# Optimization experiments

Hardware: AMD Instinct MI355X
Metric: run time of the kernel (lower is better)

## Reference

```python
import jax, jax.numpy as jnp
import numpy as np

B, CIN, COUT, T, J = 64, 128, 128, 128, 25
EPS = 1e-5  # BatchNorm2d default eps


def setup_inputs() -> dict:
    key = jax.random.key(0)
    k = jax.random.split(key, 5)
    x = jax.random.normal(k[0], (B, CIN, T, J), jnp.float32)
    adj = jax.random.normal(k[1], (J, J), jnp.float32) / np.sqrt(J).astype(np.float32)
    Wk = jax.random.normal(k[2], (COUT, CIN), jnp.float32) / np.sqrt(CIN).astype(np.float32)
    Wq = jax.random.normal(k[3], (COUT, CIN), jnp.float32) / np.sqrt(CIN).astype(np.float32)
    Ws = jax.random.normal(k[4], (COUT, CIN), jnp.float32) / np.sqrt(CIN).astype(np.float32)
    return {
        "x": x, "adj": adj,
        "Wk": Wk, "bk": jnp.zeros((COUT,), jnp.float32),
        "Wq": Wq, "bq": jnp.zeros((COUT,), jnp.float32),
        "Ws": Ws, "bs": jnp.zeros((COUT,), jnp.float32),
        "gamma": jnp.ones((COUT,), jnp.float32),
        "beta": jnp.zeros((COUT,), jnp.float32),
        "run_mean": jnp.zeros((COUT,), jnp.float32),
        "run_var": jnp.ones((COUT,), jnp.float32),
        "alpha": jnp.ones((1,), jnp.float32),
    }


def reference(x, adj, Wk, bk, Wq, bq, Ws, bs, gamma, beta, run_mean, run_var, alpha):
    # static graph conv: aggregate over joints with the shared adjacency
    static = jnp.einsum('bctj,jk->bctk', x, adj)              # [B,Cin,T,J]
    # 1x1 conv == channel matmul
    static_feat = jnp.einsum('oc,bctj->botj', Ws, static) + bs[None, :, None, None]  # [B,Cout,T,J]
    # temporal mean pooling, then key/query 1x1 convs
    x_t = x.mean(axis=2)                                      # [B,Cin,J]
    kk = jnp.einsum('oc,bcj->boj', Wk, x_t) + bk[None, :, None]  # [B,Cout,J]
    qq = jnp.einsum('oc,bcj->boj', Wq, x_t) + bq[None, :, None]  # [B,Cout,J]
    # attention-style dynamic adjacency: softmax(q^T k / sqrt(Cout)) over last axis
    scale = jnp.sqrt(jnp.asarray(kk.shape[1], x.dtype))
    scores = jnp.einsum('bcj,bck->bjk', qq, kk) / scale       # [B,J,J]
    dyn = jax.nn.softmax(scores, axis=-1)                     # [B,J,J]
    # original expands dyn to (B*T, Cout, J, J); same math without materialization:
    dyn_feat = jnp.einsum('bctj,bjk->bctk', static_feat, dyn)  # [B,Cout,T,J]
    out = static_feat + alpha[0] * dyn_feat
    # BatchNorm2d in inference mode (running stats), then ReLU
    inv = gamma[None, :, None, None] * jax.lax.rsqrt(run_var[None, :, None, None] + EPS)
    out = (out - run_mean[None, :, None, None]) * inv + beta[None, :, None, None]
    return jax.nn.relu(out)
```

## Files before the change

kernel.cpp:

```cpp
#include <hip/hip_runtime.h>

#define B_ 64
#define C_ 128
#define T_ 128
#define J_ 25
#define PIT 136
#define XP 40
#define GP 136
#define TT 4

typedef unsigned short ushort_t;
typedef __attribute__((ext_vector_type(8))) unsigned short ushort8;
typedef __attribute__((ext_vector_type(4))) unsigned short ushort4_t;
typedef __attribute__((ext_vector_type(8))) _Float16 half8;
typedef __attribute__((ext_vector_type(4))) float f32x4;

__device__ __forceinline__ float bf2f(ushort_t u) {
  unsigned int v = ((unsigned int)u) << 16;
  return __builtin_bit_cast(float, v);
}
__device__ __forceinline__ ushort_t f2bf(float f) {
  unsigned int u = __builtin_bit_cast(unsigned int, f);
  u += 0x7FFFu + ((u >> 16) & 1u);
  return (ushort_t)(u >> 16);
}
__device__ __forceinline__ ushort_t f2h_bits(float f) {
  _Float16 h = (_Float16)f;
  return __builtin_bit_cast(ushort_t, h);
}
__device__ __forceinline__ half8 cvt_bf8_h8(ushort8 u) {
  half8 r;
#pragma unroll
  for (int i = 0; i < 8; ++i) r[i] = (_Float16)bf2f(u[i]);
  return r;
}
__device__ __forceinline__ float ldv(const void* p, long i, int isf32) {
  return isf32 ? ((const float*)p)[i] : bf2f(((const ushort_t*)p)[i]);
}
__device__ __forceinline__ half8 ld8h(const void* p, long i, int isf32) {
  half8 r;
  if (isf32) {
    const float* f = (const float*)p + i;
#pragma unroll
    for (int k = 0; k < 8; ++k) r[k] = (_Float16)f[k];
  } else {
    ushort8 u = *(const ushort8*)((const ushort_t*)p + i);
    r = cvt_bf8_h8(u);
  }
  return r;
}

__global__ void k_detect(const void* __restrict__ x, int* __restrict__ flag) {
  if (threadIdx.x == 0 && blockIdx.x == 0) {
    const ushort_t* u = (const ushort_t*)x;
    int cnt = 0;
    for (int i = 0; i < 256; ++i) {
      float a = fabsf(bf2f(u[2 * i]));
      if (a > 1e-4f && a < 64.f) cnt++;
    }
    *flag = (cnt > 128) ? 0 : 1;
  }
}

__global__ __launch_bounds__(256) void k_mean(const void* __restrict__ x,
                                              float* __restrict__ xt,
                                              const int* __restrict__ flag) {
  const int isf32 = *flag;
  const int bc = blockIdx.x;
  const int b = bc >> 7, c = bc & 127;
  const long base = (long)bc * 3200;
  __shared__ float pl[3200];
  __shared__ float red[8][32];
  const int tid = threadIdx.x;
  if (isf32) {
    const f32x4* src = (const f32x4*)((const float*)x + base);
    for (int i = tid; i < 800; i += 256) *(f32x4*)&pl[i * 4] = src[i];
  } else {
    const ushort4_t* src = (const ushort4_t*)((const ushort_t*)x + base);
    for (int i = tid; i < 800; i += 256) {
      ushort4_t u = src[i];
      f32x4 v;
#pragma unroll
      for (int r = 0; r < 4; ++r) v[r] = bf2f(u[r]);
      *(f32x4*)&pl[i * 4] = v;
    }
  }
  __syncthreads();
  const int j = tid & 31, g = tid >> 5;
  float s = 0.f;
  if (j < J_) {
#pragma unroll
    for (int i = 0; i < 16; ++i) s += pl[(g * 16 + i) * 25 + j];
  }
  red[g][j] = s;
  __syncthreads();
  if (tid < 32) {
    float tot = 0.f;
#pragma unroll
    for (int gg = 0; gg < 8; ++gg) tot += red[gg][tid];
    if (tid < J_) xt[b * 4096 + tid * 128 + c] = tot * (1.0f / 128.0f);
  }
}

__global__ __launch_bounds__(256) void k_attn(
    const float* __restrict__ xt, const void* __restrict__ adj,
    const void* __restrict__ Wk, const void* __restrict__ bk,
    const void* __restrict__ Wq, const void* __restrict__ bq,
    const void* __restrict__ alphap, ushort_t* __restrict__ fkws,
    float* __restrict__ sws, const int* __restrict__ flag) {
  const int isf32 = *flag;
  const int b = blockIdx.x;
  const int tid = threadIdx.x;
  const int wv = tid >> 6, lane = tid & 63, lrow = lane & 15, quad = lane >> 4;
  const float alpha = ldv(alphap, 0, isf32);

  __shared__ __align__(16) ushort_t xtT[32 * PIT];
  __shared__ __align__(16) ushort_t kkT[32 * PIT];
  __shared__ __align__(16) ushort_t qqT[32 * PIT];
  __shared__ float sc[32 * 33];

  for (int idx = tid; idx < 32 * PIT; idx += 256) {
    int r = idx / PIT, col = idx % PIT;
    float v = (r < J_ && col < 128) ? xt[b * 4096 + r * 128 + col] : 0.f;
    xtT[idx] = f2h_bits(v);
  }
  __syncthreads();

  for (int mat = 0; mat < 2; ++mat) {
    const void* W = mat ? Wq : Wk;
    const void* bias = mat ? bq : bk;
    ushort_t* dstT = mat ? qqT : kkT;
    f32x4 acc[2][2] = {};
    for (int ks = 0; ks < 4; ++ks) {
      half8 bfr[2];
#pragma unroll
      for (int jt = 0; jt < 2; ++jt)
        bfr[jt] = *(const half8*)&xtT[(jt * 16 + lrow) * PIT + ks * 32 + quad * 8];
#pragma unroll
      for (int ot = 0; ot < 2; ++ot) {
        int o = (2 * wv + ot) * 16 + lrow;
        half8 afr = ld8h(W, o * 128 + ks * 32 + quad * 8, isf32);
#pragma unroll
        for (int jt = 0; jt < 2; ++jt)
          acc[ot][jt] = __builtin_amdgcn_mfma_f32_16x16x32_f16(afr, bfr[jt],
                                                               acc[ot][jt], 0, 0, 0);
      }
    }
#pragma unroll
    for (int ot = 0; ot < 2; ++ot) {
      int obase = (2 * wv + ot) * 16 + quad * 4;
#pragma unroll
      for (int jt = 0; jt < 2; ++jt) {
        int j = jt * 16 + lrow;
        ushort_t pack[4];
#pragma unroll
        for (int r = 0; r < 4; ++r)
          pack[r] = f2h_bits(acc[ot][jt][r] + ldv(bias, obase + r, isf32));
        *(ushort4_t*)&dstT[j * PIT + obase] = *(ushort4_t*)pack;
      }
    }
  }
  __syncthreads();

  {
    const int mt = wv >> 1, nt = wv & 1;
    f32x4 acc = {};
    for (int ks = 0; ks < 4; ++ks) {
      half8 afr = *(const half8*)&qqT[(mt * 16 + lrow) * PIT + ks * 32 + quad * 8];
      half8 bfr = *(const half8*)&kkT[(nt * 16 + lrow) * PIT + ks * 32 + quad * 8];
      acc = __builtin_amdgcn_mfma_f32_16x16x32_f16(afr, bfr, acc, 0, 0, 0);
    }
    const float rs = 0.08838834764831845f;
#pragma unroll
    for (int r = 0; r < 4; ++r)
      sc[(mt * 16 + quad * 4 + r) * 33 + nt * 16 + lrow] = acc[r] * rs;
  }
  __syncthreads();

  if (tid < J_) {
    float m = -1e30f;
    for (int k = 0; k < J_; ++k) m = fmaxf(m, sc[tid * 33 + k]);
    float sum = 0.f;
    for (int k = 0; k < J_; ++k) {
      float e = expf(sc[tid * 33 + k] - m);
      sc[tid * 33 + k] = e;
      sum += e;
    }
    float inv = 1.f / sum;
    for (int k = 0; k < J_; ++k) sc[tid * 33 + k] *= inv;
  }
  __syncthreads();

  for (int idx = tid; idx < 1280; idx += 256) {
    int k = idx / XP, jj = idx % XP;
    float v = 0.f;
    if (k < J_ && jj < J_) {
      v = ldv(adj, jj * J_ + k, isf32);
      float d = 0.f;
      for (int m = 0; m < J_; ++m) d += ldv(adj, jj * J_ + m, isf32) * sc[m * 33 + k];
      v += alpha * d;
    }
    fkws[b * 1280 + idx] = f2h_bits(v);
  }
  if (tid < 32) {
    float v = 0.f;
    if (tid < J_) {
      float d = 0.f;
      for (int jj = 0; jj < J_; ++jj) d += sc[jj * 33 + tid];
      v = 1.f + alpha * d;
    }
    sws[b * 32 + tid] = v;
  }
}

#define SM_FK 0
#define SM_X 2560
#define SM_GT 43520
#define SM_TOT 73984
__global__ __launch_bounds__(256, 2) void k_main(
    const void* __restrict__ x, const void* __restrict__ Ws,
    const void* __restrict__ bs, const void* __restrict__ gamma,
    const void* __restrict__ beta, const void* __restrict__ rmean,
    const void* __restrict__ rvar, const ushort_t* __restrict__ fkws,
    const float* __restrict__ sws, void* __restrict__ out,
    const int* __restrict__ flag) {
  const int isf32 = *flag;
  const int b = blockIdx.x >> 5, tb = blockIdx.x & 31, t0 = tb * TT;
  const int tid = threadIdx.x;
  const int wv = tid >> 6, lane = tid & 63, lrow = lane & 15, quad = lane >> 4;

  __shared__ __align__(16) char smem[SM_TOT];
  __shared__ float bnscale[128], bnshift[128], bsv[128], sv[32];
  ushort_t* fk = (ushort_t*)(smem + SM_FK);
  ushort_t* X = (ushort_t*)(smem + SM_X);
  ushort_t* gt = (ushort_t*)(smem + SM_GT);
  float* outbuf = (float*)(smem + SM_X);

  half8 wsf[2][4];
#pragma unroll
  for (int ot = 0; ot < 2; ++ot) {
    int o = (2 * wv + ot) * 16 + lrow;
#pragma unroll
    for (int ks = 0; ks < 4; ++ks)
      wsf[ot][ks] = ld8h(Ws, o * 128 + ks * 32 + quad * 8, isf32);
  }

  {
    const long fbase = ((long)(b * 128) * 128 + t0) * 25;
    if (isf32) {
      const float* xf = (const float*)x + fbase;
      for (int idx = tid; idx < 3200; idx += 256) {
        int c = idx / 25, q = idx % 25;
        f32x4 v = *(const f32x4*)(xf + (long)c * 3200 + q * 4);
#pragma unroll
        for (int r = 0; r < 4; ++r) {
          int p = q * 4 + r, tl = p / 25, j = p % 25;
          X[tl * 5120 + c * XP + j] = f2h_bits(v[r]);
        }
      }
    } else {
      const ushort_t* xh = (const ushort_t*)x + fbase;
      for (int idx = tid; idx < 3200; idx += 256) {
        int c = idx / 25, q = idx % 25;
        ushort4_t u = *(const ushort4_t*)(xh + (long)c * 3200 + q * 4);
#pragma unroll
        for (int r = 0; r < 4; ++r) {
          int p = q * 4 + r, tl = p / 25, j = p % 25;
          X[tl * 5120 + c * XP + j] = f2h_bits(bf2f(u[r]));
        }
      }
    }
    for (int idx = tid; idx < 512 * 7; idx += 256) {
      int row = idx / 7, j = 25 + idx % 7;
      X[(row >> 7) * 5120 + (row & 127) * XP + j] = 0;
    }
    for (int idx = tid; idx < 192; idx += 256) {
      int row = 100 + (idx >> 4), col8 = (idx & 15) * 8;
      half8 z = {};
      *(half8*)&gt[row * GP + col8] = z;
    }
    for (int idx = tid; idx < 1280; idx += 256) fk[idx] = fkws[b * 1280 + idx];
    if (tid < 32) sv[tid] = sws[b * 32 + tid];
    if (tid < 128) {
      float g = ldv(gamma, tid, isf32), v = ldv(rvar, tid, isf32);
      float scl = g * rsqrtf(v + 1e-5f);
      bnscale[tid] = scl;
      bnshift[tid] = ldv(beta, tid, isf32) - ldv(rmean, tid, isf32) * scl;
      bsv[tid] = ldv(bs, tid, isf32);
    }
  }
  __syncthreads();

  {
    half8 afr[2];
#pragma unroll
    for (int mt = 0; mt < 2; ++mt)
      afr[mt] = *(const half8*)&fk[(mt * 16 + lrow) * XP + quad * 8];
#pragma unroll
    for (int t = 0; t < TT; ++t) {
#pragma unroll
      for (int ci = 0; ci < 2; ++ci) {
        int ct = 2 * wv + ci;
        half8 bfr = *(const half8*)&X[t * 5120 + (ct * 16 + lrow) * XP + quad * 8];
        f32x4 accg[2] = {};
#pragma unroll
        for (int mt = 0; mt < 2; ++mt)
          accg[mt] = __builtin_amdgcn_mfma_f32_16x16x32_f16(afr[mt], bfr, accg[mt], 0, 0, 0);
#pragma unroll
        for (int mt = 0; mt < 2; ++mt)
#pragma unroll
          for (int r = 0; r < 4; ++r) {
            int kk = mt * 16 + quad * 4 + r;
            if (kk < J_)
              gt[(t * 25 + kk) * GP + ct * 16 + lrow] = f2h_bits(accg[mt][r]);
          }
      }
    }
  }
  __syncthreads();

  f32x4 acc[2][7];
#pragma unroll
  for (int ot = 0; ot < 2; ++ot)
#pragma unroll
    for (int nt = 0; nt < 7; ++nt) acc[ot][nt] = (f32x4){};
  for (int ks = 0; ks < 4; ++ks) {
    half8 bfr[7];
#pragma unroll
    for (int nt = 0; nt < 7; ++nt)
      bfr[nt] = *(const half8*)&gt[(nt * 16 + lrow) * GP + ks * 32 + quad * 8];
#pragma unroll
    for (int ot = 0; ot < 2; ++ot)
#pragma unroll
      for (int nt = 0; nt < 7; ++nt)
        acc[ot][nt] = __builtin_amdgcn_mfma_f32_16x16x32_f16(wsf[ot][ks], bfr[nt],
                                                             acc[ot][nt], 0, 0, 0);
  }
  __syncthreads();

#pragma unroll
  for (int nt = 0; nt < 7; ++nt) {
    int n = nt * 16 + lrow;
    if (n < 100) {
      float svk = sv[n % 25];
#pragma unroll
      for (int ot = 0; ot < 2; ++ot) {
        int obase = (2 * wv + ot) * 16 + quad * 4;
#pragma unroll
        for (int r = 0; r < 4; ++r) {
          int o = obase + r;
          float v = acc[ot][nt][r] + bsv[o] * svk;
          v = v * bnscale[o] + bnshift[o];
          outbuf[o * 100 + n] = fmaxf(v, 0.f);
        }
      }
    }
  }
  __syncthreads();

  {
    const long obase = ((long)(b * 128) * 128 + t0) * 25;
    if (isf32) {
      float* of = (float*)out + obase;
      for (int idx = tid; idx < 3200; idx += 256) {
        int o = idx / 25, q = idx % 25;
        *(f32x4*)(of + (long)o * 3200 + q * 4) = *(const f32x4*)&outbuf[o * 100 + q * 4];
      }
    } else {
      ushort_t* oh = (ushort_t*)out + obase;
      for (int idx = tid; idx < 3200; idx += 256) {
        int o = idx / 25, q = idx % 25;
        f32x4 v = *(const f32x4*)&outbuf[o * 100 + q * 4];
        ushort4_t u;
#pragma unroll
        for (int r = 0; r < 4; ++r) u[r] = f2bf(v[r]);
        *(ushort4_t*)(oh + (long)o * 3200 + q * 4) = u;
      }
    }
  }
}

extern "C" void kernel_launch(void* const* d_in, const int* in_sizes, int n_in,
                              void* d_out, int out_size, void* d_ws, size_t ws_size,
                              hipStream_t stream) {
  const void* x = d_in[0];
  const void* adj = d_in[1];
  const void* Wk = d_in[2];
  const void* bk = d_in[3];
  const void* Wq = d_in[4];
  const void* bq = d_in[5];
  const void* Ws = d_in[6];
  const void* bsp = d_in[7];
  const void* gamma = d_in[8];
  const void* beta = d_in[9];
  const void* rmean = d_in[10];
  const void* rvar = d_in[11];
  const void* alphap = d_in[12];

  char* ws = (char*)d_ws;
  int* flag = (int*)ws;
  float* xt = (float*)(ws + 256);
  ushort_t* fkws = (ushort_t*)(ws + 256 + 64 * 4096 * 4);
  float* sws = (float*)(ws + 256 + 64 * 4096 * 4 + 64 * 1280 * 2);

  k_detect<<<1, 64, 0, stream>>>(x, flag);
  k_mean<<<B_ * C_, 256, 0, stream>>>(x, xt, flag);
  k_attn<<<B_, 256, 0, stream>>>(xt, adj, Wk, bk, Wq, bq, alphap, fkws, sws, flag);
  k_main<<<B_ * (T_ / TT), 256, 0, stream>>>(x, Ws, bsp, gamma, beta, rmean, rvar,
                                             fkws, sws, d_out, flag);
}
```

Baseline: 319.0 us.

## Load x fragments directly from global in k_main and shrink LDS to raise occupancy

Removes the separate dtype-detect kernel and replaces it with a per-block ballot-based detection. In k_main, the staging of the x tile into LDS is dropped, and MFMA B fragments are read directly from global memory with unaligned vector loads. The output buffer is stored as fp16 in LDS, which shrinks shared memory from ~74KB to ~33KB so the kernel can run 4 blocks per CU instead of 2. The risk is less-coalesced global loads, and fp16 intermediate rounding of the outputs.

Result: faster. 298.4 us (-6.5%).

```diff
diff --git a/kernel.cpp b/kernel.cpp
--- a/kernel.cpp
+++ b/kernel.cpp
@@ -14,6 +14,8 @@
 typedef __attribute__((ext_vector_type(4))) unsigned short ushort4_t;
 typedef __attribute__((ext_vector_type(8))) _Float16 half8;
 typedef __attribute__((ext_vector_type(4))) float f32x4;
+typedef float f32x4u __attribute__((ext_vector_type(4), aligned(4)));
+typedef unsigned short ushort8u __attribute__((ext_vector_type(8), aligned(2)));
 
 __device__ __forceinline__ float bf2f(ushort_t u) {
   unsigned int v = ((unsigned int)u) << 16;
@@ -28,6 +30,9 @@
   _Float16 h = (_Float16)f;
   return __builtin_bit_cast(ushort_t, h);
 }
+__device__ __forceinline__ float h2f(ushort_t u) {
+  return (float)__builtin_bit_cast(_Float16, u);
+}
 __device__ __forceinline__ half8 cvt_bf8_h8(ushort8 u) {
   half8 r;
 #pragma unroll
@@ -50,28 +55,23 @@
   return r;
 }
 
-__global__ void k_detect(const void* __restrict__ x, int* __restrict__ flag) {
-  if (threadIdx.x == 0 && blockIdx.x == 0) {
-    const ushort_t* u = (const ushort_t*)x;
-    int cnt = 0;
-    for (int i = 0; i < 256; ++i) {
-      float a = fabsf(bf2f(u[2 * i]));
-      if (a > 1e-4f && a < 64.f) cnt++;
-    }
-    *flag = (cnt > 128) ? 0 : 1;
-  }
+__device__ __forceinline__ int detect_isf32(const void* p, int tid) {
+  const ushort_t* u = (const ushort_t*)p;
+  float a = fabsf(bf2f(u[2 * (tid & 63)]));
+  int ok = (a > 1e-4f && a < 64.f) ? 1 : 0;
+  unsigned long long m = __ballot(ok);
+  return (__popcll(m) > 32) ? 0 : 1;
 }
 
 __global__ __launch_bounds__(256) void k_mean(const void* __restrict__ x,
-                                              float* __restrict__ xt,
-                                              const int* __restrict__ flag) {
-  const int isf32 = *flag;
+                                              float* __restrict__ xt) {
   const int bc = blockIdx.x;
   const int b = bc >> 7, c = bc & 127;
   const long base = (long)bc * 3200;
+  const int tid = threadIdx.x;
+  const int isf32 = detect_isf32((const ushort_t*)x + base, tid);
   __shared__ float pl[3200];
   __shared__ float red[8][32];
-  const int tid = threadIdx.x;
   if (isf32) {
     const f32x4* src = (const f32x4*)((const float*)x + base);
     for (int i = tid; i < 800; i += 256) *(f32x4*)&pl[i * 4] = src[i];
@@ -107,10 +107,10 @@
     const void* __restrict__ Wk, const void* __restrict__ bk,
     const void* __restrict__ Wq, const void* __restrict__ bq,
     const void* __restrict__ alphap, ushort_t* __restrict__ fkws,
-    float* __restrict__ sws, const int* __restrict__ flag) {
-  const int isf32 = *flag;
+    float* __restrict__ sws) {
   const int b = blockIdx.x;
   const int tid = threadIdx.x;
+  const int isf32 = detect_isf32(Wk, tid);
   const int wv = tid >> 6, lane = tid & 63, lrow = lane & 15, quad = lane >> 4;
   const float alpha = ldv(alphap, 0, isf32);
 
@@ -214,27 +214,24 @@
 }
 
 #define SM_FK 0
-#define SM_X 2560
-#define SM_GT 43520
-#define SM_TOT 73984
-__global__ __launch_bounds__(256, 2) void k_main(
+#define SM_GT 2560
+#define SM_TOT 33024
+__global__ __launch_bounds__(256, 4) void k_main(
     const void* __restrict__ x, const void* __restrict__ Ws,
     const void* __restrict__ bs, const void* __restrict__ gamma,
     const void* __restrict__ beta, const void* __restrict__ rmean,
     const void* __restrict__ rvar, const ushort_t* __restrict__ fkws,
-    const float* __restrict__ sws, void* __restrict__ out,
-    const int* __restrict__ flag) {
-  const int isf32 = *flag;
+    const float* __restrict__ sws, void* __restrict__ out) {
+  const int tid = threadIdx.x;
+  const int isf32 = detect_isf32(Ws, tid);
   const int b = blockIdx.x >> 5, tb = blockIdx.x & 31, t0 = tb * TT;
-  const int tid = threadIdx.x;
   const int wv = tid >> 6, lane = tid & 63, lrow = lane & 15, quad = lane >> 4;
 
   __shared__ __align__(16) char smem[SM_TOT];
   __shared__ float bnscale[128], bnshift[128], bsv[128], sv[32];
   ushort_t* fk = (ushort_t*)(smem + SM_FK);
-  ushort_t* X = (ushort_t*)(smem + SM_X);
   ushort_t* gt = (ushort_t*)(smem + SM_GT);
-  float* outbuf = (float*)(smem + SM_X);
+  ushort_t* outbuf = (ushort_t*)(smem + SM_GT);
 
   half8 wsf[2][4];
 #pragma unroll
@@ -245,49 +242,20 @@
       wsf[ot][ks] = ld8h(Ws, o * 128 + ks * 32 + quad * 8, isf32);
   }
 
-  {
-    const long fbase = ((long)(b * 128) * 128 + t0) * 25;
-    if (isf32) {
-      const float* xf = (const float*)x + fbase;
-      for (int idx = tid; idx < 3200; idx += 256) {
-        int c = idx / 25, q = idx % 25;
-        f32x4 v = *(const f32x4*)(xf + (long)c * 3200 + q * 4);
-#pragma unroll
-        for (int r = 0; r < 4; ++r) {
-          int p = q * 4 + r, tl = p / 25, j = p % 25;
-          X[tl * 5120 + c * XP + j] = f2h_bits(v[r]);
-        }
-      }
-    } else {
-      const ushort_t* xh = (const ushort_t*)x + fbase;
-      for (int idx = tid; idx < 3200; idx += 256) {
-        int c = idx / 25, q = idx % 25;
-        ushort4_t u = *(const ushort4_t*)(xh + (long)c * 3200 + q * 4);
-#pragma unroll
-        for (int r = 0; r < 4; ++r) {
-          int p = q * 4 + r, tl = p / 25, j = p % 25;
-          X[tl * 5120 + c * XP + j] = f2h_bits(bf2f(u[r]));
-        }
-      }
-    }
-    for (int idx = tid; idx < 512 * 7; idx += 256) {
-      int row = idx / 7, j = 25 + idx % 7;
-      X[(row >> 7) * 5120 + (row & 127) * XP + j] = 0;
-    }
-    for (int idx = tid; idx < 192; idx += 256) {
-      int row = 100 + (idx >> 4), col8 = (idx & 15) * 8;
-      half8 z = {};
-      *(half8*)&gt[row * GP + col8] = z;
-    }
-    for (int idx = tid; idx < 1280; idx += 256) fk[idx] = fkws[b * 1280 + idx];
-    if (tid < 32) sv[tid] = sws[b * 32 + tid];
-    if (tid < 128) {
-      float g = ldv(gamma, tid, isf32), v = ldv(rvar, tid, isf32);
-      float scl = g * rsqrtf(v + 1e-5f);
-      bnscale[tid] = scl;
-      bnshift[tid] = ldv(beta, tid, isf32) - ldv(rmean, tid, isf32) * scl;
-      bsv[tid] = ldv(bs, tid, isf32);
-    }
+  for (int i = tid; i < 160; i += 256)
+    *(ushort8*)&fk[i * 8] = *(const ushort8*)&fkws[b * 1280 + i * 8];
+  for (int i = tid; i < 204; i += 256) {
+    int row = 100 + i / 17, col8 = (i % 17) * 8;
+    ushort8 z = {};
+    *(ushort8*)&gt[row * GP + col8] = z;
+  }
+  if (tid < 32) sv[tid] = sws[b * 32 + tid];
+  if (tid < 128) {
+    float g = ldv(gamma, tid, isf32), v = ldv(rvar, tid, isf32);
+    float scl = g * rsqrtf(v + 1e-5f);
+    bnscale[tid] = scl;
+    bnshift[tid] = ldv(beta, tid, isf32) - ldv(rmean, tid, isf32) * scl;
+    bsv[tid] = ldv(bs, tid, isf32);
   }
   __syncthreads();
 
@@ -296,12 +264,33 @@
 #pragma unroll
     for (int mt = 0; mt < 2; ++mt)
       afr[mt] = *(const half8*)&fk[(mt * 16 + lrow) * XP + quad * 8];
+    const float* xf = (const float*)x;
+    const ushort_t* xh = (const ushort_t*)x;
 #pragma unroll
     for (int t = 0; t < TT; ++t) {
 #pragma unroll
       for (int ci = 0; ci < 2; ++ci) {
         int ct = 2 * wv + ci;
-        half8 bfr = *(const half8*)&X[t * 5120 + (ct * 16 + lrow) * XP + quad * 8];
+        long p = (long)b * 409600 + (long)(ct * 16 + lrow) * 3200 + (t0 + t) * 25;
+        half8 bfr;
+        if (quad < 3) {
+          if (isf32) {
+            f32x4u v0 = *(const f32x4u*)(xf + p + quad * 8);
+            f32x4u v1 = *(const f32x4u*)(xf + p + quad * 8 + 4);
+#pragma unroll
+            for (int r = 0; r < 4; ++r) {
+              bfr[r] = (_Float16)v0[r];
+              bfr[4 + r] = (_Float16)v1[r];
+            }
+          } else {
+            ushort8u u = *(const ushort8u*)(xh + p + quad * 8);
+#pragma unroll
+            for (int r = 0; r < 8; ++r) bfr[r] = (_Float16)bf2f(u[r]);
+          }
+        } else {
+          bfr = (half8){};
+          bfr[0] = (_Float16)(isf32 ? xf[p + 24] : bf2f(xh[p + 24]));
+        }
         f32x4 accg[2] = {};
 #pragma unroll
         for (int mt = 0; mt < 2; ++mt)
@@ -325,16 +314,14 @@
 #pragma unroll
     for (int nt = 0; nt < 7; ++nt) acc[ot][nt] = (f32x4){};
   for (int ks = 0; ks < 4; ++ks) {
-    half8 bfr[7];
-#pragma unroll
-    for (int nt = 0; nt < 7; ++nt)
-      bfr[nt] = *(const half8*)&gt[(nt * 16 + lrow) * GP + ks * 32 + quad * 8];
-#pragma unroll
-    for (int ot = 0; ot < 2; ++ot)
-#pragma unroll
-      for (int nt = 0; nt < 7; ++nt)
-        acc[ot][nt] = __builtin_amdgcn_mfma_f32_16x16x32_f16(wsf[ot][ks], bfr[nt],
+#pragma unroll
+    for (int nt = 0; nt < 7; ++nt) {
+      half8 bfr = *(const half8*)&gt[(nt * 16 + lrow) * GP + ks * 32 + quad * 8];
+#pragma unroll
+      for (int ot = 0; ot < 2; ++ot)
+        acc[ot][nt] = __builtin_amdgcn_mfma_f32_16x16x32_f16(wsf[ot][ks], bfr,
                                                              acc[ot][nt], 0, 0, 0);
+    }
   }
   __syncthreads();
 
@@ -351,7 +338,7 @@
           int o = obase + r;
           float v = acc[ot][nt][r] + bsv[o] * svk;
           v = v * bnscale[o] + bnshift[o];
-          outbuf[o * 100 + n] = fmaxf(v, 0.f);
+          outbuf[o * 100 + n] = f2h_bits(fmaxf(v, 0.f));
         }
       }
     }
@@ -364,17 +351,21 @@
       float* of = (float*)out + obase;
       for (int idx = tid; idx < 3200; idx += 256) {
         int o = idx / 25, q = idx % 25;
-        *(f32x4*)(of + (long)o * 3200 + q * 4) = *(const f32x4*)&outbuf[o * 100 + q * 4];
+        ushort4_t u = *(const ushort4_t*)&outbuf[o * 100 + q * 4];
+        f32x4 v;
+#pragma unroll
+        for (int r = 0; r < 4; ++r) v[r] = h2f(u[r]);
+        *(f32x4*)(of + (long)o * 3200 + q * 4) = v;
       }
     } else {
       ushort_t* oh = (ushort_t*)out + obase;
       for (int idx = tid; idx < 3200; idx += 256) {
         int o = idx / 25, q = idx % 25;
-        f32x4 v = *(const f32x4*)&outbuf[o * 100 + q * 4];
-        ushort4_t u;
-#pragma unroll
-        for (int r = 0; r < 4; ++r) u[r] = f2bf(v[r]);
-        *(ushort4_t*)(oh + (long)o * 3200 + q * 4) = u;
+        ushort4_t u = *(const ushort4_t*)&outbuf[o * 100 + q * 4];
+        ushort4_t w;
+#pragma unroll
+        for (int r = 0; r < 4; ++r) w[r] = f2bf(h2f(u[r]));
+        *(ushort4_t*)(oh + (long)o * 3200 + q * 4) = w;
       }
     }
   }
@@ -398,14 +389,12 @@
   const void* alphap = d_in[12];
 
   char* ws = (char*)d_ws;
-  int* flag = (int*)ws;
-  float* xt = (float*)(ws + 256);
-  ushort_t* fkws = (ushort_t*)(ws + 256 + 64 * 4096 * 4);
-  float* sws = (float*)(ws + 256 + 64 * 4096 * 4 + 64 * 1280 * 2);
-
-  k_detect<<<1, 64, 0, stream>>>(x, flag);
-  k_mean<<<B_ * C_, 256, 0, stream>>>(x, xt, flag);
-  k_attn<<<B_, 256, 0, stream>>>(xt, adj, Wk, bk, Wq, bq, alphap, fkws, sws, flag);
+  float* xt = (float*)ws;
+  ushort_t* fkws = (ushort_t*)(ws + 64 * 4096 * 4);
+  float* sws = (float*)(ws + 64 * 4096 * 4 + 64 * 1280 * 2);
+
+  k_mean<<<B_ * C_, 256, 0, stream>>>(x, xt);
+  k_attn<<<B_, 256, 0, stream>>>(xt, adj, Wk, bk, Wq, bq, alphap, fkws, sws);
   k_main<<<B_ * (T_ / TT), 256, 0, stream>>>(x, Ws, bsp, gamma, beta, rmean, rvar,
-                                             fkws, sws, d_out, flag);
-}
+                                             fkws, sws, d_out);
+}
```
